# Performance work log

Measured on AMD Instinct MI355X. Metric: run time of the kernel, lower is better.

The kernel has to match this reference:

```python
import jax, jax.numpy as jnp
import numpy as np

N_NODES = 50000
NUM_REL = 8
IN_DIM = 128
HID = 256
NUM_CLASSES = 2
E = 1600000
M = 200000
LN_EPS = 1e-5


def setup_inputs() -> dict:
    key = jax.random.key(0)
    ks = jax.random.split(key, 20)
    s = 0.05
    inp = {
        "x": jax.random.normal(ks[0], (N_NODES, IN_DIM), jnp.float32),
        "edge_index": jax.random.randint(ks[1], (2, E), 0, N_NODES, jnp.int32),
        "edge_type": jax.random.randint(ks[2], (E,), 0, NUM_REL, jnp.int32),
        "dec_edges": jax.random.randint(ks[3], (M, 2), 0, N_NODES, jnp.int32),
        # conv1
        "W1": jax.random.normal(ks[4], (NUM_REL, IN_DIM, HID), jnp.float32) * s,
        "root1": jax.random.normal(ks[5], (IN_DIM, HID), jnp.float32) * s,
        "b1": jnp.zeros((HID,), jnp.float32),
        # conv2
        "W2": jax.random.normal(ks[6], (NUM_REL, HID, HID), jnp.float32) * s,
        "root2": jax.random.normal(ks[7], (HID, HID), jnp.float32) * s,
        "b2": jnp.zeros((HID,), jnp.float32),
        # layernorms
        "ln1_g": jnp.ones((HID,), jnp.float32),
        "ln1_b": jnp.zeros((HID,), jnp.float32),
        "ln2_g": jnp.ones((HID,), jnp.float32),
        "ln2_b": jnp.zeros((HID,), jnp.float32),
        # edge MLP: 2*HID -> HID -> HID//2 -> NUM_CLASSES
        "mlp_w1": jax.random.normal(ks[8], (2 * HID, HID), jnp.float32) * s,
        "mlp_b1": jnp.zeros((HID,), jnp.float32),
        "mlp_w2": jax.random.normal(ks[9], (HID, HID // 2), jnp.float32) * s,
        "mlp_b2": jnp.zeros((HID // 2,), jnp.float32),
        "mlp_w3": jax.random.normal(ks[10], (HID // 2, NUM_CLASSES), jnp.float32) * s,
        "mlp_b3": jnp.zeros((NUM_CLASSES,), jnp.float32),
    }
    return inp


def layer_norm(h, g, b):
    mu = jnp.mean(h, axis=-1, keepdims=True)
    var = jnp.mean(jnp.square(h - mu), axis=-1, keepdims=True)
    return (h - mu) * jax.lax.rsqrt(var + LN_EPS) * g + b


def rgcn_conv(x, edge_index, edge_type, W, root, bias):
    # PyG RGCNConv with aggr='mean': per-relation mean aggregation of
    # neighbor features, aggregate-then-transform (valid since linear),
    # plus root transform and bias.
    src, dst = edge_index[0], edge_index[1]
    xs = x[src]  # [E, d_in]
    out = x @ root + bias
    num_rel = W.shape[0]
    for r in range(num_rel):
        m = (edge_type == r).astype(x.dtype)  # [E]
        agg = jax.ops.segment_sum(xs * m[:, None], dst, num_segments=x.shape[0])
        cnt = jax.ops.segment_sum(m, dst, num_segments=x.shape[0])
        out = out + (agg / jnp.maximum(cnt, 1.0)[:, None]) @ W[r]
    return out


def reference(x, edge_index, edge_type, dec_edges,
              W1, root1, b1, W2, root2, b2,
              ln1_g, ln1_b, ln2_g, ln2_b,
              mlp_w1, mlp_b1, mlp_w2, mlp_b2, mlp_w3, mlp_b3):
    # encode (dropout is identity in eval mode)
    h1 = rgcn_conv(x, edge_index, edge_type, W1, root1, b1)
    h1 = layer_norm(jax.nn.relu(h1), ln1_g, ln1_b)
    h2 = rgcn_conv(h1, edge_index, edge_type, W2, root2, b2)
    h2 = layer_norm(jax.nn.relu(h2), ln2_g, ln2_b)
    h = h1 + h2
    # decode: gather endpoints, concat, MLP (exact-erf GELU as nn.GELU)
    z = jnp.concatenate([h[dec_edges[:, 0]], h[dec_edges[:, 1]]], axis=1)
    z = jax.nn.gelu(z @ mlp_w1 + mlp_b1, approximate=False)
    z = jax.nn.gelu(z @ mlp_w2 + mlp_b2, approximate=False)
    return z @ mlp_w3 + mlp_b3
```

## Files before the change

### kernel.cpp

```cpp
#include <hip/hip_runtime.h>
#include <math.h>

typedef __attribute__((ext_vector_type(8))) short short8;
typedef __attribute__((ext_vector_type(4))) float f32x4;
typedef __attribute__((address_space(3))) void lds_void;
typedef const __attribute__((address_space(1))) void glb_void;

#define N_NODES 50000
#define NUM_REL 8
#define IN_DIM 128
#define HID 256
#define E_EDGES 1600000
#define M_DEC 200000
#define K1 1152
#define K2 2304
#define LN_EPS 1e-5f
#define NSEG (N_NODES * 8)
#define NB2 782
#define SA_WG 391
#define SA_CH 4096
#define SA_DCH 512

__device__ __forceinline__ float b2f(ushort u) {
    union { unsigned int i; float f; } v; v.i = ((unsigned int)u) << 16; return v.f;
}
__device__ __forceinline__ ushort f2b(float f) {
    union { float f; unsigned int i; } v; v.f = f;
    unsigned int r = v.i + 0x7FFFu + ((v.i >> 16) & 1u);
    return (ushort)(r >> 16);
}
__device__ __forceinline__ unsigned int pk2(ushort a, ushort b) {
    return (unsigned int)a | ((unsigned int)b << 16);
}
__device__ __forceinline__ float gelu_fast(float x) {
    float y = 1.5957691216f * (x + 0.044715f * x * x * x);
    float e = __expf(y);
    float t = 1.f - 2.f * __builtin_amdgcn_rcpf(e + 1.f);
    return 0.5f * x * (1.f + t);
}
__device__ __forceinline__ int clampn(int v) {
    if ((unsigned)v >= N_NODES) v = (v < 0) ? 0 : N_NODES - 1;
    return v;
}


__global__ __launch_bounds__(256) void coarse_count(const int* __restrict__ ei,
                                                    const int* __restrict__ dec,
                                                    int* __restrict__ bh, int* __restrict__ dh) {
    __shared__ int lb[NB2], ld[NB2];
    const int t = threadIdx.x;
    for (int i = t; i < NB2; i += 256) { lb[i] = 0; ld[i] = 0; }
    __syncthreads();
    const int e0 = blockIdx.x * SA_CH;
#pragma unroll
    for (int k = 0; k < 16; ++k) {
        int e = e0 + k * 256 + t;
        if (e < E_EDGES) {
            int dst = clampn(ei[E_EDGES + e]);
            atomicAdd(&lb[dst >> 6], 1);
        }
    }
    const int d0 = blockIdx.x * SA_DCH;
#pragma unroll
    for (int k = 0; k < 2; ++k) {
        int i = d0 + k * 256 + t;
        if (i < M_DEC) {
            int a = clampn(dec[(size_t)i * 2]);
            atomicAdd(&ld[a >> 6], 1);
        }
    }
    __syncthreads();
    for (int i = t; i < NB2; i += 256) {
        if (lb[i]) atomicAdd(&bh[i], lb[i]);
        if (ld[i]) atomicAdd(&dh[i], ld[i]);
    }
}

__global__ __launch_bounds__(1024) void scan_buckets(const int* __restrict__ bh, int* __restrict__ bbase,
                                                     int* __restrict__ bcur,
                                                     const int* __restrict__ dh, int* __restrict__ dbase,
                                                     int* __restrict__ dcur, int* __restrict__ rp2) {
    __shared__ int ts[1024];
    const int t = threadIdx.x;
    const int* src = (blockIdx.x == 0) ? bh : dh;
    int* ob = (blockIdx.x == 0) ? bbase : dbase;
    int* oc = (blockIdx.x == 0) ? bcur : dcur;
    int v = (t < NB2) ? src[t] : 0;
    ts[t] = v;
    __syncthreads();
#pragma unroll
    for (int off = 1; off < 1024; off <<= 1) {
        int u = (t >= off) ? ts[t - off] : 0;
        __syncthreads();
        ts[t] += u;
        __syncthreads();
    }
    if (t < NB2) { int ex = ts[t] - v; ob[t] = ex; oc[t] = ex; }
    if (t == NB2 - 1) ob[NB2] = ts[t];
    if (t == 0 && blockIdx.x == 0) rp2[NSEG] = E_EDGES;
}

__global__ __launch_bounds__(256) void stageA(const int* __restrict__ ei, const int* __restrict__ et,
                                              int* __restrict__ bcur, unsigned int* __restrict__ sbuf,
                                              const int* __restrict__ dec, int* __restrict__ dcur,
                                              int* __restrict__ perm) {
    __shared__ int h[NB2], base_[NB2];
    const int t = threadIdx.x;
    const int e0 = blockIdx.x * SA_CH;
    for (int i = t; i < NB2; i += 256) h[i] = 0;
    __syncthreads();
    int myb[16];
#pragma unroll
    for (int k = 0; k < 16; ++k) {
        int e = e0 + k * 256 + t;
        int b = -1;
        if (e < E_EDGES) {
            int dst = clampn(ei[E_EDGES + e]);
            b = dst >> 6;
            atomicAdd(&h[b], 1);
        }
        myb[k] = b;
    }
    __syncthreads();
    for (int i = t; i < NB2; i += 256) {
        int c = h[i];
        base_[i] = c ? atomicAdd(&bcur[i], c) : 0;
    }
    __syncthreads();
    for (int i = t; i < NB2; i += 256) h[i] = 0;
    __syncthreads();
#pragma unroll
    for (int k = 0; k < 16; ++k) {
        int e = e0 + k * 256 + t;
        int b = myb[k];
        if (b >= 0) {
            int dst = clampn(ei[E_EDGES + e]);
            int src = clampn(ei[e]);
            int r = et[e] & 7;
            int off = atomicAdd(&h[b], 1);
            sbuf[base_[b] + off] =
                (unsigned)src | ((unsigned)r << 16) | ((unsigned)(dst & 63) << 19);
        }
    }
    __syncthreads();
    for (int i = t; i < NB2; i += 256) h[i] = 0;
    __syncthreads();
    const int d0 = blockIdx.x * SA_DCH;
    int dbk[2];
#pragma unroll
    for (int k = 0; k < 2; ++k) {
        int i = d0 + k * 256 + t;
        int b = -1;
        if (i < M_DEC) {
            int a = clampn(dec[(size_t)i * 2]);
            b = a >> 6;
            atomicAdd(&h[b], 1);
        }
        dbk[k] = b;
    }
    __syncthreads();
    for (int i = t; i < NB2; i += 256) {
        int c = h[i];
        base_[i] = c ? atomicAdd(&dcur[i], c) : 0;
    }
    __syncthreads();
    for (int i = t; i < NB2; i += 256) h[i] = 0;
    __syncthreads();
#pragma unroll
    for (int k = 0; k < 2; ++k) {
        int i = d0 + k * 256 + t;
        int b = dbk[k];
        if (b >= 0) {
            int off = atomicAdd(&h[b], 1);
            perm[base_[b] + off] = i;
        }
    }
}

__global__ __launch_bounds__(512) void stageB(const unsigned int* __restrict__ sbuf,
                                              const int* __restrict__ bbase,
                                              int* __restrict__ rp2,
                                              unsigned int* __restrict__ epk) {
    __shared__ int cnt[512];
    __shared__ int pref[512];
    const int t = threadIdx.x;
    const int b = blockIdx.x;
    const int s0 = bbase[b], s1 = bbase[b + 1];
    cnt[t] = 0;
    __syncthreads();
    for (int i = s0 + t; i < s1; i += 512) {
        unsigned int p = sbuf[i];
        int ls = (((p >> 19) & 63) << 3) | ((p >> 16) & 7);
        atomicAdd(&cnt[ls], 1);
    }
    __syncthreads();
    pref[t] = cnt[t];
    __syncthreads();
#pragma unroll
    for (int off = 1; off < 512; off <<= 1) {
        int u = (t >= off) ? pref[t - off] : 0;
        __syncthreads();
        pref[t] += u;
        __syncthreads();
    }
    int excl = pref[t] - cnt[t];
    int seg = b * 512 + t;
    if (seg < NSEG) rp2[seg] = s0 + excl;
    __syncthreads();
    pref[t] = excl;
    cnt[t] = 0;
    __syncthreads();
    for (int i = s0 + t; i < s1; i += 512) {
        unsigned int p = sbuf[i];
        int ls = (((p >> 19) & 63) << 3) | ((p >> 16) & 7);
        int off = atomicAdd(&cnt[ls], 1);
        epk[s0 + pref[ls] + off] = p & 0xFFFFu;
    }
}

__global__ void pack_all(const float* __restrict__ x, ushort* __restrict__ xb,
                         const float* __restrict__ root1, const float* __restrict__ W1,
                         const float* __restrict__ root2, const float* __restrict__ W2,
                         ushort* __restrict__ B1t, ushort* __restrict__ B2t,
                         const float* __restrict__ mw1, const float* __restrict__ mw2,
                         ushort* __restrict__ wuvt, ushort* __restrict__ w2t) {
    const int XC = N_NODES * IN_DIM / 4;
    const int N1 = HID * K1;
    const int N2 = HID * K2;
    const int NU = 512 * 256;
    const int NW = 128 * 256;
    int idx = blockIdx.x * 256 + threadIdx.x;
    if (idx < XC) {
        float4 v = *(const float4*)(x + (size_t)idx * 4);
        uint2 o;
        o.x = pk2(f2b(v.x), f2b(v.y));
        o.y = pk2(f2b(v.z), f2b(v.w));
        *(uint2*)(xb + (size_t)idx * 4) = o;
        return;
    }
    idx -= XC;
    if (idx < N1) {
        int n = idx / K1, k = idx % K1;
        float v;
        if (k < IN_DIM) v = root1[k * HID + n];
        else { int kk = k - IN_DIM; v = W1[(size_t)(kk >> 7) * IN_DIM * HID + (kk & 127) * HID + n]; }
        B1t[(size_t)n * K1 + k] = f2b(v);
        return;
    }
    idx -= N1;
    if (idx < N2) {
        int n = idx / K2, k = idx % K2;
        float v;
        if (k < HID) v = root2[k * HID + n];
        else { int kk = k - HID; v = W2[(size_t)(kk >> 8) * HID * HID + (kk & 255) * HID + n]; }
        B2t[(size_t)n * K2 + k] = f2b(v);
        return;
    }
    idx -= N2;
    if (idx < NU) {
        int n = idx / 256, k = idx % 256;
        float v = (n < 256) ? mw1[(size_t)k * 256 + n] : mw1[(size_t)(256 + k) * 256 + (n - 256)];
        wuvt[(size_t)n * 256 + k] = f2b(v);
        return;
    }
    idx -= NU;
    if (idx < NW) {
        int n = idx / 256, k = idx % 256;
        w2t[n * 256 + k] = f2b(mw2[k * 128 + n]);
    }
}


#define FL1() { int c_ = segend - segbeg; float inv_ = c_ > 0 ? 1.f / (float)c_ : 0.f; \
    *(unsigned int*)(Arow + IN_DIM + r * IN_DIM + 2 * lane) = \
        pk2(f2b((aA.x + aB.x) * inv_), f2b((aA.y + aB.y) * inv_)); \
    aA.x = 0.f; aA.y = 0.f; aB.x = 0.f; aB.y = 0.f; \
    ++r; segbeg = segend; segend = (r < 8) ? rp[r + 1] : end; \
    if (segend < segbeg) segend = segbeg; if (segend > end) segend = end; }
#define CK1(EI) { while (r < 8 && (EI) >= segend) FL1(); }
#define AC1A(U) { aA.x += b2f((ushort)((U) & 0xFFFFu)); aA.y += b2f((ushort)((U) >> 16)); }
#define AC1B(U) { aB.x += b2f((ushort)((U) & 0xFFFFu)); aB.y += b2f((ushort)((U) >> 16)); }

__global__ __launch_bounds__(256) void agg1_kernel(const ushort* __restrict__ xb,
                                                   const int* __restrict__ rp2,
                                                   const unsigned int* __restrict__ epk,
                                                   ushort* __restrict__ Achunk, int n0, int m) {
    const int w = threadIdx.x >> 6, lane = threadIdx.x & 63;
    const int local = blockIdx.x * 4 + w;
    if (local >= m) return;
    const int n = n0 + local;
    const int* rp = rp2 + n * 8;
    ushort* Arow = Achunk + (size_t)local * K1;
    const ushort* xbb = xb + 2 * lane;
    *(unsigned int*)(Arow + 2 * lane) = *(const unsigned int*)(xb + (size_t)n * IN_DIM + 2 * lane);

    int beg = rp[0], end = rp[8];
    if (beg < 0) beg = 0;
    if (end > E_EDGES) end = E_EDGES;
    if (end < beg) end = beg;

    float2 aA = {0.f, 0.f}, aB = {0.f, 0.f};
    int r = 0, segbeg = beg, segend = rp[1];
    if (segend < segbeg) segend = segbeg; if (segend > end) segend = end;

    int e = beg;
    for (; e + 7 < end; e += 8) {
        unsigned int p0 = epk[e],     p1 = epk[e + 1], p2 = epk[e + 2], p3 = epk[e + 3];
        unsigned int p4 = epk[e + 4], p5 = epk[e + 5], p6 = epk[e + 6], p7 = epk[e + 7];
        unsigned int u0 = *(const unsigned int*)(xbb + (size_t)p0 * IN_DIM);
        unsigned int u1 = *(const unsigned int*)(xbb + (size_t)p1 * IN_DIM);
        unsigned int u2 = *(const unsigned int*)(xbb + (size_t)p2 * IN_DIM);
        unsigned int u3 = *(const unsigned int*)(xbb + (size_t)p3 * IN_DIM);
        unsigned int u4 = *(const unsigned int*)(xbb + (size_t)p4 * IN_DIM);
        unsigned int u5 = *(const unsigned int*)(xbb + (size_t)p5 * IN_DIM);
        unsigned int u6 = *(const unsigned int*)(xbb + (size_t)p6 * IN_DIM);
        unsigned int u7 = *(const unsigned int*)(xbb + (size_t)p7 * IN_DIM);
        CK1(e)     AC1A(u0) CK1(e + 1) AC1B(u1)
        CK1(e + 2) AC1A(u2) CK1(e + 3) AC1B(u3)
        CK1(e + 4) AC1A(u4) CK1(e + 5) AC1B(u5)
        CK1(e + 6) AC1A(u6) CK1(e + 7) AC1B(u7)
    }
    for (; e < end; ++e) {
        unsigned int p = epk[e];
        unsigned int u = *(const unsigned int*)(xbb + (size_t)p * IN_DIM);
        CK1(e) AC1A(u)
    }
    while (r < 8) FL1();
}

#define FL2() { int c_ = segend - segbeg; float inv_ = c_ > 0 ? 1.f / (float)c_ : 0.f; \
    f32x4 t_ = aA + aB; uint2 o_; \
    o_.x = pk2(f2b(t_[0] * inv_), f2b(t_[1] * inv_)); \
    o_.y = pk2(f2b(t_[2] * inv_), f2b(t_[3] * inv_)); \
    *(uint2*)(Arow + HID + r * HID + 4 * lane) = o_; \
    aA = (f32x4){0.f, 0.f, 0.f, 0.f}; aB = aA; \
    ++r; segbeg = segend; segend = (r < 8) ? rp[r + 1] : end; \
    if (segend < segbeg) segend = segbeg; if (segend > end) segend = end; }
#define CK2(EI) { while (r < 8 && (EI) >= segend) FL2(); }
#define AC2A(U) { f32x4 f_; \
    f_[0] = b2f((ushort)((U).x & 0xFFFFu)); f_[1] = b2f((ushort)((U).x >> 16)); \
    f_[2] = b2f((ushort)((U).y & 0xFFFFu)); f_[3] = b2f((ushort)((U).y >> 16)); aA += f_; }
#define AC2B(U) { f32x4 f_; \
    f_[0] = b2f((ushort)((U).x & 0xFFFFu)); f_[1] = b2f((ushort)((U).x >> 16)); \
    f_[2] = b2f((ushort)((U).y & 0xFFFFu)); f_[3] = b2f((ushort)((U).y >> 16)); aB += f_; }

__global__ __launch_bounds__(256) void agg2_kernel(const ushort* __restrict__ h1,
                                                   const int* __restrict__ rp2,
                                                   const unsigned int* __restrict__ epk,
                                                   ushort* __restrict__ Achunk, int n0, int m) {
    const int w = threadIdx.x >> 6, lane = threadIdx.x & 63;
    const int local = blockIdx.x * 4 + w;
    if (local >= m) return;
    const int n = n0 + local;
    const int* rp = rp2 + n * 8;
    ushort* Arow = Achunk + (size_t)local * K2;
    const ushort* hb = h1 + 4 * lane;
    *(uint2*)(Arow + 4 * lane) = *(const uint2*)(h1 + (size_t)n * HID + 4 * lane);

    int beg = rp[0], end = rp[8];
    if (beg < 0) beg = 0;
    if (end > E_EDGES) end = E_EDGES;
    if (end < beg) end = beg;

    f32x4 aA = {0.f, 0.f, 0.f, 0.f}, aB = {0.f, 0.f, 0.f, 0.f};
    int r = 0, segbeg = beg, segend = rp[1];
    if (segend < segbeg) segend = segbeg; if (segend > end) segend = end;

    int e = beg;
    for (; e + 7 < end; e += 8) {
        unsigned int p0 = epk[e],     p1 = epk[e + 1], p2 = epk[e + 2], p3 = epk[e + 3];
        unsigned int p4 = epk[e + 4], p5 = epk[e + 5], p6 = epk[e + 6], p7 = epk[e + 7];
        uint2 u0 = *(const uint2*)(hb + (size_t)p0 * HID);
        uint2 u1 = *(const uint2*)(hb + (size_t)p1 * HID);
        uint2 u2 = *(const uint2*)(hb + (size_t)p2 * HID);
        uint2 u3 = *(const uint2*)(hb + (size_t)p3 * HID);
        uint2 u4 = *(const uint2*)(hb + (size_t)p4 * HID);
        uint2 u5 = *(const uint2*)(hb + (size_t)p5 * HID);
        uint2 u6 = *(const uint2*)(hb + (size_t)p6 * HID);
        uint2 u7 = *(const uint2*)(hb + (size_t)p7 * HID);
        CK2(e)     AC2A(u0) CK2(e + 1) AC2B(u1)
        CK2(e + 2) AC2A(u2) CK2(e + 3) AC2B(u3)
        CK2(e + 4) AC2A(u4) CK2(e + 5) AC2B(u5)
        CK2(e + 6) AC2A(u6) CK2(e + 7) AC2B(u7)
    }
    for (; e < end; ++e) {
        unsigned int p = epk[e];
        uint2 u = *(const uint2*)(hb + (size_t)p * HID);
        CK2(e) AC2A(u)
    }
    while (r < 8) FL2();
}


#define STAGE(BUF, KO) { \
    __builtin_amdgcn_global_load_lds((glb_void*)(Ab + (KO)), \
        (lds_void*)(AsBase + (BUF) * 4096 + wave * 8 * 64), 16, 0, 0); \
    _Pragma("unroll") \
    for (int j_ = 0; j_ < 4; ++j_) \
        __builtin_amdgcn_global_load_lds((glb_void*)(Bb + (size_t)j_ * 8 * K + (KO)), \
            (lds_void*)(BsBase + (BUF) * 16384 + (wave * 32 + j_ * 8) * 64), 16, 0, 0); }

#define COMPUTE(CUR) { \
    _Pragma("unroll") \
    for (int kk = 0; kk < 2; ++kk) { \
        const int gsw = (((kk * 4 + qd) ^ (cc & 7)) * 8); \
        short8 af[2], bfv[4]; \
        _Pragma("unroll") \
        for (int i = 0; i < 2; ++i) \
            af[i] = *(const short8*)&AsBase[(CUR) * 4096 + (mh * 32 + i * 16 + cc) * 64 + gsw]; \
        _Pragma("unroll") \
        for (int j = 0; j < 4; ++j) \
            bfv[j] = *(const short8*)&BsBase[(CUR) * 16384 + (wn + j * 16 + cc) * 64 + gsw]; \
        _Pragma("unroll") \
        for (int i = 0; i < 2; ++i) \
            _Pragma("unroll") \
            for (int j = 0; j < 4; ++j) \
                acc[i][j] = __builtin_amdgcn_mfma_f32_16x16x32_bf16(af[i], bfv[j], acc[i][j], 0, 0, 0); \
    } }

__global__ __launch_bounds__(512, 4) void gemm_fused(
    const ushort* __restrict__ A, const ushort* __restrict__ Bt,
    int lda, int M, int K,
    const float* __restrict__ bias, const float* __restrict__ g,
    const float* __restrict__ bvec, const ushort* __restrict__ resid,
    ushort* __restrict__ outp, int ldc, int rowOff) {
    __shared__ __align__(16) ushort smem[40960];
    ushort* AsBase = smem;
    ushort* BsBase = smem + 2 * 64 * 64;
    const int tid = threadIdx.x;
    const int wave = tid >> 6, lane = tid & 63;
    const int w4 = wave & 3, mh = wave >> 2;
    const int cc = lane & 15, qd = lane >> 4;
    const int row0 = blockIdx.x * 64;
    const int colBase = blockIdx.y * 256;
    const int wn = w4 * 64;
    const int srow = lane >> 3;
    const int sgrp = (lane & 7) ^ (srow & 7);
    f32x4 acc[2][4];
#pragma unroll
    for (int i = 0; i < 2; ++i)
#pragma unroll
        for (int j = 0; j < 4; ++j) acc[i][j] = (f32x4){0.f, 0.f, 0.f, 0.f};

    const ushort* Ab = A + (size_t)(row0 + wave * 8 + srow) * lda + sgrp * 8;
    const ushort* Bb = Bt + (size_t)(colBase + wave * 32 + srow) * K + sgrp * 8;

    STAGE(0, 0)
    for (int k0 = 0; k0 < K; k0 += 128) {
        if (k0 + 64 < K) {
            STAGE(1, k0 + 64)
            asm volatile("s_waitcnt vmcnt(5)" ::: "memory");
        } else {
            asm volatile("s_waitcnt vmcnt(0)" ::: "memory");
        }
        __builtin_amdgcn_s_barrier();
        COMPUTE(0)
        asm volatile("s_waitcnt lgkmcnt(0)" ::: "memory");
        __builtin_amdgcn_s_barrier();

        if (k0 + 128 < K) {
            STAGE(0, k0 + 128)
            asm volatile("s_waitcnt vmcnt(5)" ::: "memory");
        } else {
            asm volatile("s_waitcnt vmcnt(0)" ::: "memory");
        }
        __builtin_amdgcn_s_barrier();
        COMPUTE(1)
        asm volatile("s_waitcnt lgkmcnt(0)" ::: "memory");
        __builtin_amdgcn_s_barrier();
    }

    if (g) {
        float* partS = (float*)smem;
        float* partQ = (float*)smem + 256;
        float* muS   = (float*)smem + 512;
        float* rsS   = (float*)smem + 576;
#pragma unroll
        for (int j = 0; j < 4; ++j) {
            float bcol = bias[wn + j * 16 + cc];
#pragma unroll
            for (int i = 0; i < 2; ++i)
#pragma unroll
                for (int r = 0; r < 4; ++r)
                    acc[i][j][r] = fmaxf(acc[i][j][r] + bcol, 0.f);
        }
#pragma unroll
        for (int i = 0; i < 2; ++i)
#pragma unroll
            for (int r = 0; r < 4; ++r) {
                float s = acc[i][0][r] + acc[i][1][r] + acc[i][2][r] + acc[i][3][r];
                float q = acc[i][0][r] * acc[i][0][r] + acc[i][1][r] * acc[i][1][r]
                        + acc[i][2][r] * acc[i][2][r] + acc[i][3][r] * acc[i][3][r];
#pragma unroll
                for (int off = 1; off <= 8; off <<= 1) {
                    s += __shfl_xor(s, off, 64);
                    q += __shfl_xor(q, off, 64);
                }
                if (cc == 0) {
                    int row = mh * 32 + i * 16 + qd * 4 + r;
                    partS[row * 4 + w4] = s;
                    partQ[row * 4 + w4] = q;
                }
            }
        __syncthreads();
        if (tid < 64) {
            float S = partS[tid * 4] + partS[tid * 4 + 1] + partS[tid * 4 + 2] + partS[tid * 4 + 3];
            float Q = partQ[tid * 4] + partQ[tid * 4 + 1] + partQ[tid * 4 + 2] + partQ[tid * 4 + 3];
            float mu = S * (1.f / 256.f);
            float var = Q * (1.f / 256.f) - mu * mu;
            muS[tid] = mu;
            rsS[tid] = rsqrtf(fmaxf(var, 0.f) + LN_EPS);
        }
        __syncthreads();
#pragma unroll
        for (int i = 0; i < 2; ++i)
#pragma unroll
            for (int r = 0; r < 4; ++r) {
                int row = mh * 32 + i * 16 + qd * 4 + r;
                int grow = row0 + row;
                if (grow >= M) continue;
                float mu = muS[row], rs = rsS[row];
                size_t base = (size_t)(rowOff + grow) * ldc;
#pragma unroll
                for (int j = 0; j < 4; ++j) {
                    int col = wn + j * 16 + cc;
                    float val = (acc[i][j][r] - mu) * rs * g[col] + bvec[col];
                    if (resid) val += b2f(resid[base + col]);
                    outp[base + col] = f2b(val);
                }
            }
    } else {
#pragma unroll
        for (int i = 0; i < 2; ++i)
#pragma unroll
            for (int r = 0; r < 4; ++r) {
                int grow = row0 + mh * 32 + i * 16 + qd * 4 + r;
                if (grow >= M) continue;
                size_t base = (size_t)(rowOff + grow) * ldc;
#pragma unroll
                for (int j = 0; j < 4; ++j) {
                    int col = colBase + wn + j * 16 + cc;
                    outp[base + col] = f2b(acc[i][j][r]);
                }
            }
    }
}

__global__ __launch_bounds__(256) void edge_kernel(
    const ushort* __restrict__ uv, const int* __restrict__ dec, const int* __restrict__ perm,
    const float* __restrict__ b1, const ushort* __restrict__ w2t,
    const float* __restrict__ b2, const float* __restrict__ w3,
    const float* __restrict__ b3, float* __restrict__ outp, int M) {
    __shared__ __align__(16) ushort z1s[64][264];
    __shared__ __align__(16) ushort z2s[64][136];
    __shared__ float b1s[256], b2s[128], w3s[256];
    const int tid = threadIdx.x;
    const int wave = tid >> 6, lane = tid & 63;
    const int cc = lane & 15, qd = lane >> 4, lk = qd * 8, rr = qd * 4;
    const int e0 = blockIdx.x * 64;

    b1s[tid] = b1[tid];
    if (tid < 128) b2s[tid] = b2[tid];
    w3s[tid] = w3[tid];
    __syncthreads();

    {
        int e = tid >> 2, seg = tid & 3;
        int ge = perm[e0 + e];
        if (ge < 0) ge = 0; if (ge >= M) ge = M - 1;
        int a = dec[(size_t)ge * 2];
        int b = dec[(size_t)ge * 2 + 1];
        if (a < 0) a = 0; if (a >= N_NODES) a = N_NODES - 1;
        if (b < 0) b = 0; if (b >= N_NODES) b = N_NODES - 1;
        const ushort* up = uv + (size_t)a * 512 + seg * 64;
        const ushort* vp = uv + (size_t)b * 512 + 256 + seg * 64;
        short8 us[8], vs[8];
#pragma unroll
        for (int j = 0; j < 8; ++j) us[j] = *(const short8*)(up + j * 8);
#pragma unroll
        for (int j = 0; j < 8; ++j) vs[j] = *(const short8*)(vp + j * 8);
        int d0 = seg * 64;
#pragma unroll
        for (int j = 0; j < 8; ++j) {
            int d = d0 + j * 8;
            short8 zs;
#pragma unroll
            for (int l = 0; l < 8; ++l) {
                float z = b2f((ushort)us[j][l]) + b2f((ushort)vs[j][l]) + b1s[d + l];
                zs[l] = (short)f2b(gelu_fast(z));
            }
            *(short8*)&z1s[e][d] = zs;
        }
    }
    __syncthreads();

    f32x4 acc[4][2];
#pragma unroll
    for (int i = 0; i < 4; ++i)
#pragma unroll
        for (int j = 0; j < 2; ++j) acc[i][j] = (f32x4){0.f, 0.f, 0.f, 0.f};
    const int n0 = wave * 32;
#pragma unroll
    for (int ks = 0; ks < 8; ++ks) {
        short8 af[4], bfv[2];
#pragma unroll
        for (int i = 0; i < 4; ++i) af[i] = *(const short8*)&z1s[i * 16 + cc][ks * 32 + lk];
#pragma unroll
        for (int j = 0; j < 2; ++j)
            bfv[j] = *(const short8*)(w2t + (size_t)(n0 + j * 16 + cc) * 256 + ks * 32 + lk);
#pragma unroll
        for (int i = 0; i < 4; ++i)
#pragma unroll
            for (int j = 0; j < 2; ++j)
                acc[i][j] = __builtin_amdgcn_mfma_f32_16x16x32_bf16(af[i], bfv[j], acc[i][j], 0, 0, 0);
    }
#pragma unroll
    for (int i = 0; i < 4; ++i)
#pragma unroll
        for (int j = 0; j < 2; ++j)
#pragma unroll
            for (int r = 0; r < 4; ++r) {
                int m = i * 16 + rr + r;
                int n = n0 + j * 16 + cc;
                z2s[m][n] = f2b(gelu_fast(acc[i][j][r] + b2s[n]));
            }
    __syncthreads();

    if (tid < 128) {
        int e = tid >> 1, c = tid & 1;
        float s = b3[c];
        for (int k = 0; k < 128; ++k) s += b2f(z2s[e][k]) * w3s[k * 2 + c];
        int ge = perm[e0 + e];
        if (ge >= 0 && ge < M) outp[(size_t)ge * 2 + c] = s;
    }
}

extern "C" void kernel_launch(void* const* d_in, const int* in_sizes, int n_in,
                              void* d_out, int out_size, void* d_ws, size_t ws_size,
                              hipStream_t stream) {
    const float* x          = (const float*)d_in[0];
    const int*   edge_index = (const int*)d_in[1];
    const int*   edge_type  = (const int*)d_in[2];
    const int*   dec_edges  = (const int*)d_in[3];
    const float* W1         = (const float*)d_in[4];
    const float* root1      = (const float*)d_in[5];
    const float* b1         = (const float*)d_in[6];
    const float* W2         = (const float*)d_in[7];
    const float* root2      = (const float*)d_in[8];
    const float* b2         = (const float*)d_in[9];
    const float* ln1_g      = (const float*)d_in[10];
    const float* ln1_b      = (const float*)d_in[11];
    const float* ln2_g      = (const float*)d_in[12];
    const float* ln2_b      = (const float*)d_in[13];
    const float* mlp_w1     = (const float*)d_in[14];
    const float* mlp_b1     = (const float*)d_in[15];
    const float* mlp_w2     = (const float*)d_in[16];
    const float* mlp_b2     = (const float*)d_in[17];
    const float* mlp_w3     = (const float*)d_in[18];
    const float* mlp_b3     = (const float*)d_in[19];

    char* ws = (char*)d_ws;
    size_t off = 0;
    auto alloc = [&](size_t bytes) {
        void* p = ws + off;
        off += (bytes + 255) & ~(size_t)255;
        return p;
    };
    unsigned int* epk     = (unsigned int*)alloc((size_t)E_EDGES * 4);
    unsigned int* sbuf    = (unsigned int*)alloc((size_t)E_EDGES * 4);
    int*          rp2     = (int*)alloc((size_t)(NSEG + 1) * 4);
    int*          hz      = (int*)alloc((size_t)2 * NB2 * 4);
    int*          bh      = hz;
    int*          dh      = hz + NB2;
    int*          bbase   = (int*)alloc((size_t)(NB2 + 1) * 4);
    int*          dbase   = (int*)alloc((size_t)(NB2 + 1) * 4);
    int*          bcur    = (int*)alloc((size_t)NB2 * 4);
    int*          dcur    = (int*)alloc((size_t)NB2 * 4);
    int*          perm    = (int*)alloc((size_t)M_DEC * 4);
    ushort*       B1t     = (ushort*)alloc((size_t)HID * K1 * 2);
    ushort*       B2t     = (ushort*)alloc((size_t)HID * K2 * 2);
    ushort*       wuvt    = (ushort*)alloc((size_t)512 * 256 * 2);
    ushort*       w2t     = (ushort*)alloc((size_t)128 * 256 * 2);
    ushort*       xb      = (ushort*)alloc((size_t)N_NODES * IN_DIM * 2);
    ushort*       hfin    = (ushort*)alloc((size_t)N_NODES * HID * 2);

    size_t regionOff = off;
    ushort* h1ln  = (ushort*)(ws + regionOff);
    ushort* uvbuf = h1ln;
    size_t h1b = (((size_t)N_NODES * HID * 2) + 255) & ~(size_t)255;
    ushort* Achunk = (ushort*)(ws + regionOff + h1b);
    long long chunkB = (long long)ws_size - (long long)(regionOff + h1b);
    int chunk = 64;
    if (chunkB > 0) {
        long long c = chunkB / ((long long)K2 * 2);
        if (c > N_NODES) c = N_NODES;
        c &= ~63LL;
        if (c >= 64) chunk = (int)c;
    }
    int chunk1 = chunk * 2;
    if (chunk1 > N_NODES) chunk1 = N_NODES;

    hipMemsetAsync(hz, 0, (size_t)2 * NB2 * 4, stream);
    coarse_count<<<SA_WG, 256, 0, stream>>>(edge_index, dec_edges, bh, dh);
    scan_buckets<<<2, 1024, 0, stream>>>(bh, bbase, bcur, dh, dbase, dcur, rp2);
    stageA<<<SA_WG, 256, 0, stream>>>(edge_index, edge_type, bcur, sbuf, dec_edges, dcur, perm);
    stageB<<<NB2, 512, 0, stream>>>(sbuf, bbase, rp2, epk);

    {
        int total = N_NODES * IN_DIM / 4 + HID * K1 + HID * K2 + 512 * 256 + 128 * 256;
        pack_all<<<(total + 255) / 256, 256, 0, stream>>>(x, xb, root1, W1, root2, W2,
                                                          B1t, B2t, mlp_w1, mlp_w2, wuvt, w2t);
    }

    for (int n0 = 0; n0 < N_NODES; n0 += chunk1) {
        int m = N_NODES - n0; if (m > chunk1) m = chunk1;
        agg1_kernel<<<(m + 3) / 4, 256, 0, stream>>>(xb, rp2, epk, Achunk, n0, m);
        gemm_fused<<<dim3((m + 63) / 64, 1), 512, 0, stream>>>(
            Achunk, B1t, K1, m, K1, b1, ln1_g, ln1_b, nullptr, h1ln, HID, n0);
    }
    for (int n0 = 0; n0 < N_NODES; n0 += chunk) {
        int m = N_NODES - n0; if (m > chunk) m = chunk;
        agg2_kernel<<<(m + 3) / 4, 256, 0, stream>>>(h1ln, rp2, epk, Achunk, n0, m);
        gemm_fused<<<dim3((m + 63) / 64, 1), 512, 0, stream>>>(
            Achunk, B2t, K2, m, K2, b2, ln2_g, ln2_b, h1ln, hfin, HID, n0);
    }

    gemm_fused<<<dim3((N_NODES + 63) / 64, 2), 512, 0, stream>>>(
        hfin, wuvt, HID, N_NODES, HID, nullptr, nullptr, nullptr, nullptr, uvbuf, 512, 0);

    edge_kernel<<<(M_DEC + 63) / 64, 256, 0, stream>>>(
        uvbuf, dec_edges, perm, mlp_b1, w2t, mlp_b2, mlp_w3, mlp_b3, (float*)d_out, M_DEC);
}
```

Baseline: 704.3 us.

## Triple-buffer GEMM K-loop and widen gather unroll in aggregation kernels

The fused GEMM moves from a double-buffered to a triple-buffered LDS pipeline. Two K-tiles are prefetched ahead of compute, with the wait threshold raised to match, and the launch-bounds occupancy hint drops from 4 to 2. Both aggregation kernels get a 16-wide gather unroll ahead of the existing 8-wide loop, plus an occupancy hint of 6, to keep more neighbour loads in flight. The trade-off is that the GEMM's shared memory grows to about 120 KB per block, which likely allows only one resident block per CU. That cuts the latency hiding that came from running several blocks at once, and the larger unroll raises register pressure in the aggregation kernels.

```diff
diff --git a/kernel.cpp b/kernel.cpp
--- a/kernel.cpp
+++ b/kernel.cpp
@@ -281,10 +281,10 @@
 #define AC1A(U) { aA.x += b2f((ushort)((U) & 0xFFFFu)); aA.y += b2f((ushort)((U) >> 16)); }
 #define AC1B(U) { aB.x += b2f((ushort)((U) & 0xFFFFu)); aB.y += b2f((ushort)((U) >> 16)); }
 
-__global__ __launch_bounds__(256) void agg1_kernel(const ushort* __restrict__ xb,
-                                                   const int* __restrict__ rp2,
-                                                   const unsigned int* __restrict__ epk,
-                                                   ushort* __restrict__ Achunk, int n0, int m) {
+__global__ __launch_bounds__(256, 6) void agg1_kernel(const ushort* __restrict__ xb,
+                                                      const int* __restrict__ rp2,
+                                                      const unsigned int* __restrict__ epk,
+                                                      ushort* __restrict__ Achunk, int n0, int m) {
     const int w = threadIdx.x >> 6, lane = threadIdx.x & 63;
     const int local = blockIdx.x * 4 + w;
     if (local >= m) return;
@@ -304,6 +304,36 @@
     if (segend < segbeg) segend = segbeg; if (segend > end) segend = end;
 
     int e = beg;
+    for (; e + 15 < end; e += 16) {
+        unsigned int p0 = epk[e],      p1 = epk[e + 1],  p2 = epk[e + 2],  p3 = epk[e + 3];
+        unsigned int p4 = epk[e + 4],  p5 = epk[e + 5],  p6 = epk[e + 6],  p7 = epk[e + 7];
+        unsigned int p8 = epk[e + 8],  p9 = epk[e + 9],  pa = epk[e + 10], pb = epk[e + 11];
+        unsigned int pc = epk[e + 12], pd = epk[e + 13], pe = epk[e + 14], pf = epk[e + 15];
+        unsigned int u0 = *(const unsigned int*)(xbb + (size_t)p0 * IN_DIM);
+        unsigned int u1 = *(const unsigned int*)(xbb + (size_t)p1 * IN_DIM);
+        unsigned int u2 = *(const unsigned int*)(xbb + (size_t)p2 * IN_DIM);
+        unsigned int u3 = *(const unsigned int*)(xbb + (size_t)p3 * IN_DIM);
+        unsigned int u4 = *(const unsigned int*)(xbb + (size_t)p4 * IN_DIM);
+        unsigned int u5 = *(const unsigned int*)(xbb + (size_t)p5 * IN_DIM);
+        unsigned int u6 = *(const unsigned int*)(xbb + (size_t)p6 * IN_DIM);
+        unsigned int u7 = *(const unsigned int*)(xbb + (size_t)p7 * IN_DIM);
+        unsigned int u8 = *(const unsigned int*)(xbb + (size_t)p8 * IN_DIM);
+        unsigned int u9 = *(const unsigned int*)(xbb + (size_t)p9 * IN_DIM);
+        unsigned int ua = *(const unsigned int*)(xbb + (size_t)pa * IN_DIM);
+        unsigned int ub = *(const unsigned int*)(xbb + (size_t)pb * IN_DIM);
+        unsigned int uc = *(const unsigned int*)(xbb + (size_t)pc * IN_DIM);
+        unsigned int ud = *(const unsigned int*)(xbb + (size_t)pd * IN_DIM);
+        unsigned int ue = *(const unsigned int*)(xbb + (size_t)pe * IN_DIM);
+        unsigned int uf = *(const unsigned int*)(xbb + (size_t)pf * IN_DIM);
+        CK1(e)      AC1A(u0) CK1(e + 1)  AC1B(u1)
+        CK1(e + 2)  AC1A(u2) CK1(e + 3)  AC1B(u3)
+        CK1(e + 4)  AC1A(u4) CK1(e + 5)  AC1B(u5)
+        CK1(e + 6)  AC1A(u6) CK1(e + 7)  AC1B(u7)
+        CK1(e + 8)  AC1A(u8) CK1(e + 9)  AC1B(u9)
+        CK1(e + 10) AC1A(ua) CK1(e + 11) AC1B(ub)
+        CK1(e + 12) AC1A(uc) CK1(e + 13) AC1B(ud)
+        CK1(e + 14) AC1A(ue) CK1(e + 15) AC1B(uf)
+    }
     for (; e + 7 < end; e += 8) {
         unsigned int p0 = epk[e],     p1 = epk[e + 1], p2 = epk[e + 2], p3 = epk[e + 3];
         unsigned int p4 = epk[e + 4], p5 = epk[e + 5], p6 = epk[e + 6], p7 = epk[e + 7];
@@ -344,10 +374,10 @@
     f_[0] = b2f((ushort)((U).x & 0xFFFFu)); f_[1] = b2f((ushort)((U).x >> 16)); \
     f_[2] = b2f((ushort)((U).y & 0xFFFFu)); f_[3] = b2f((ushort)((U).y >> 16)); aB += f_; }
 
-__global__ __launch_bounds__(256) void agg2_kernel(const ushort* __restrict__ h1,
-                                                   const int* __restrict__ rp2,
-                                                   const unsigned int* __restrict__ epk,
-                                                   ushort* __restrict__ Achunk, int n0, int m) {
+__global__ __launch_bounds__(256, 6) void agg2_kernel(const ushort* __restrict__ h1,
+                                                      const int* __restrict__ rp2,
+                                                      const unsigned int* __restrict__ epk,
+                                                      ushort* __restrict__ Achunk, int n0, int m) {
     const int w = threadIdx.x >> 6, lane = threadIdx.x & 63;
     const int local = blockIdx.x * 4 + w;
     if (local >= m) return;
@@ -367,6 +397,36 @@
     if (segend < segbeg) segend = segbeg; if (segend > end) segend = end;
 
     int e = beg;
+    for (; e + 15 < end; e += 16) {
+        unsigned int p0 = epk[e],      p1 = epk[e + 1],  p2 = epk[e + 2],  p3 = epk[e + 3];
+        unsigned int p4 = epk[e + 4],  p5 = epk[e + 5],  p6 = epk[e + 6],  p7 = epk[e + 7];
+        unsigned int p8 = epk[e + 8],  p9 = epk[e + 9],  pa = epk[e + 10], pb = epk[e + 11];
+        unsigned int pc = epk[e + 12], pd = epk[e + 13], pe = epk[e + 14], pf = epk[e + 15];
+        uint2 u0 = *(const uint2*)(hb + (size_t)p0 * HID);
+        uint2 u1 = *(const uint2*)(hb + (size_t)p1 * HID);
+        uint2 u2 = *(const uint2*)(hb + (size_t)p2 * HID);
+        uint2 u3 = *(const uint2*)(hb + (size_t)p3 * HID);
+        uint2 u4 = *(const uint2*)(hb + (size_t)p4 * HID);
+        uint2 u5 = *(const uint2*)(hb + (size_t)p5 * HID);
+        uint2 u6 = *(const uint2*)(hb + (size_t)p6 * HID);
+        uint2 u7 = *(const uint2*)(hb + (size_t)p7 * HID);
+        uint2 u8 = *(const uint2*)(hb + (size_t)p8 * HID);
+        uint2 u9 = *(const uint2*)(hb + (size_t)p9 * HID);
+        uint2 ua = *(const uint2*)(hb + (size_t)pa * HID);
+        uint2 ub = *(const uint2*)(hb + (size_t)pb * HID);
+        uint2 uc = *(const uint2*)(hb + (size_t)pc * HID);
+        uint2 ud = *(const uint2*)(hb + (size_t)pd * HID);
+        uint2 ue = *(const uint2*)(hb + (size_t)pe * HID);
+        uint2 uf = *(const uint2*)(hb + (size_t)pf * HID);
+        CK2(e)      AC2A(u0) CK2(e + 1)  AC2B(u1)
+        CK2(e + 2)  AC2A(u2) CK2(e + 3)  AC2B(u3)
+        CK2(e + 4)  AC2A(u4) CK2(e + 5)  AC2B(u5)
+        CK2(e + 6)  AC2A(u6) CK2(e + 7)  AC2B(u7)
+        CK2(e + 8)  AC2A(u8) CK2(e + 9)  AC2B(u9)
+        CK2(e + 10) AC2A(ua) CK2(e + 11) AC2B(ub)
+        CK2(e + 12) AC2A(uc) CK2(e + 13) AC2B(ud)
+        CK2(e + 14) AC2A(ue) CK2(e + 15) AC2B(uf)
+    }
     for (; e + 7 < end; e += 8) {
         unsigned int p0 = epk[e],     p1 = epk[e + 1], p2 = epk[e + 2], p3 = epk[e + 3];
         unsigned int p4 = epk[e + 4], p5 = epk[e + 5], p6 = epk[e + 6], p7 = epk[e + 7];
@@ -418,15 +478,27 @@
                 acc[i][j] = __builtin_amdgcn_mfma_f32_16x16x32_bf16(af[i], bfv[j], acc[i][j], 0, 0, 0); \
     } }
 
-__global__ __launch_bounds__(512, 4) void gemm_fused(
+#define PHASE(BUF, KCUR, KPRE) { \
+    if ((KPRE) < K) { \
+        STAGE(((BUF) + 2) % 3, (KPRE)) \
+        asm volatile("s_waitcnt vmcnt(10)" ::: "memory"); \
+    } else { \
+        asm volatile("s_waitcnt vmcnt(0)" ::: "memory"); \
+    } \
+    __builtin_amdgcn_s_barrier(); \
+    COMPUTE(BUF) \
+    asm volatile("s_waitcnt lgkmcnt(0)" ::: "memory"); \
+    __builtin_amdgcn_s_barrier(); }
+
+__global__ __launch_bounds__(512, 2) void gemm_fused(
     const ushort* __restrict__ A, const ushort* __restrict__ Bt,
     int lda, int M, int K,
     const float* __restrict__ bias, const float* __restrict__ g,
     const float* __restrict__ bvec, const ushort* __restrict__ resid,
     ushort* __restrict__ outp, int ldc, int rowOff) {
-    __shared__ __align__(16) ushort smem[40960];
+    __shared__ __align__(16) ushort smem[61440];
     ushort* AsBase = smem;
-    ushort* BsBase = smem + 2 * 64 * 64;
+    ushort* BsBase = smem + 3 * 64 * 64;
     const int tid = threadIdx.x;
     const int wave = tid >> 6, lane = tid & 63;
     const int w4 = wave & 3, mh = wave >> 2;
@@ -446,28 +518,13 @@
     const ushort* Bb = Bt + (size_t)(colBase + wave * 32 + srow) * K + sgrp * 8;
 
     STAGE(0, 0)
-    for (int k0 = 0; k0 < K; k0 += 128) {
-        if (k0 + 64 < K) {
-            STAGE(1, k0 + 64)
-            asm volatile("s_waitcnt vmcnt(5)" ::: "memory");
-        } else {
-            asm volatile("s_waitcnt vmcnt(0)" ::: "memory");
-        }
-        __builtin_amdgcn_s_barrier();
-        COMPUTE(0)
-        asm volatile("s_waitcnt lgkmcnt(0)" ::: "memory");
-        __builtin_amdgcn_s_barrier();
-
-        if (k0 + 128 < K) {
-            STAGE(0, k0 + 128)
-            asm volatile("s_waitcnt vmcnt(5)" ::: "memory");
-        } else {
-            asm volatile("s_waitcnt vmcnt(0)" ::: "memory");
-        }
-        __builtin_amdgcn_s_barrier();
-        COMPUTE(1)
-        asm volatile("s_waitcnt lgkmcnt(0)" ::: "memory");
-        __builtin_amdgcn_s_barrier();
+    if (64 < K) STAGE(1, 64)
+    for (int k0 = 0; k0 < K; k0 += 192) {
+        PHASE(0, k0, k0 + 128)
+        if (k0 + 64 >= K) break;
+        PHASE(1, k0 + 64, k0 + 192)
+        if (k0 + 128 >= K) break;
+        PHASE(2, k0 + 128, k0 + 256)
     }
 
     if (g) {
```

Result: slower. 746.8 us (+6.0%).

## Overlap next-chunk aggregation with current-chunk GEMM in one fused launch

Applied to the files above, without the earlier changes.

The aggregation and GEMM paths are split into device functions. A combined kernel now assigns its first blocks to the GEMM on the current chunk and its remaining blocks to aggregating the next chunk into a second buffer, so memory-bound gathers run alongside MFMA work. Chunk size is capped and the workspace is double-buffered. Launch bounds for the GEMM drop from 4 to 2 blocks per CU, which loosens register limits but may reduce occupancy. The fused kernel also carries a larger shared allocation into the aggregation blocks.

```diff
diff --git a/kernel.cpp b/kernel.cpp
--- a/kernel.cpp
+++ b/kernel.cpp
@@ -281,16 +281,11 @@
 #define AC1A(U) { aA.x += b2f((ushort)((U) & 0xFFFFu)); aA.y += b2f((ushort)((U) >> 16)); }
 #define AC1B(U) { aB.x += b2f((ushort)((U) & 0xFFFFu)); aB.y += b2f((ushort)((U) >> 16)); }
 
-__global__ __launch_bounds__(256) void agg1_kernel(const ushort* __restrict__ xb,
-                                                   const int* __restrict__ rp2,
-                                                   const unsigned int* __restrict__ epk,
-                                                   ushort* __restrict__ Achunk, int n0, int m) {
-    const int w = threadIdx.x >> 6, lane = threadIdx.x & 63;
-    const int local = blockIdx.x * 4 + w;
-    if (local >= m) return;
-    const int n = n0 + local;
+__device__ __forceinline__ void agg1_node(const ushort* __restrict__ xb,
+                                          const int* __restrict__ rp2,
+                                          const unsigned int* __restrict__ epk,
+                                          ushort* __restrict__ Arow, int n, int lane) {
     const int* rp = rp2 + n * 8;
-    ushort* Arow = Achunk + (size_t)local * K1;
     const ushort* xbb = xb + 2 * lane;
     *(unsigned int*)(Arow + 2 * lane) = *(const unsigned int*)(xb + (size_t)n * IN_DIM + 2 * lane);
 
@@ -344,16 +339,11 @@
     f_[0] = b2f((ushort)((U).x & 0xFFFFu)); f_[1] = b2f((ushort)((U).x >> 16)); \
     f_[2] = b2f((ushort)((U).y & 0xFFFFu)); f_[3] = b2f((ushort)((U).y >> 16)); aB += f_; }
 
-__global__ __launch_bounds__(256) void agg2_kernel(const ushort* __restrict__ h1,
-                                                   const int* __restrict__ rp2,
-                                                   const unsigned int* __restrict__ epk,
-                                                   ushort* __restrict__ Achunk, int n0, int m) {
-    const int w = threadIdx.x >> 6, lane = threadIdx.x & 63;
-    const int local = blockIdx.x * 4 + w;
-    if (local >= m) return;
-    const int n = n0 + local;
+__device__ __forceinline__ void agg2_node(const ushort* __restrict__ h1,
+                                          const int* __restrict__ rp2,
+                                          const unsigned int* __restrict__ epk,
+                                          ushort* __restrict__ Arow, int n, int lane) {
     const int* rp = rp2 + n * 8;
-    ushort* Arow = Achunk + (size_t)local * K2;
     const ushort* hb = h1 + 4 * lane;
     *(uint2*)(Arow + 4 * lane) = *(const uint2*)(h1 + (size_t)n * HID + 4 * lane);
 
@@ -389,6 +379,26 @@
         CK2(e) AC2A(u)
     }
     while (r < 8) FL2();
+}
+
+__global__ __launch_bounds__(256) void agg1_kernel(const ushort* __restrict__ xb,
+                                                   const int* __restrict__ rp2,
+                                                   const unsigned int* __restrict__ epk,
+                                                   ushort* __restrict__ Achunk, int n0, int m) {
+    const int w = threadIdx.x >> 6, lane = threadIdx.x & 63;
+    const int local = blockIdx.x * 4 + w;
+    if (local >= m) return;
+    agg1_node(xb, rp2, epk, Achunk + (size_t)local * K1, n0 + local, lane);
+}
+
+__global__ __launch_bounds__(256) void agg2_kernel(const ushort* __restrict__ h1,
+                                                   const int* __restrict__ rp2,
+                                                   const unsigned int* __restrict__ epk,
+                                                   ushort* __restrict__ Achunk, int n0, int m) {
+    const int w = threadIdx.x >> 6, lane = threadIdx.x & 63;
+    const int local = blockIdx.x * 4 + w;
+    if (local >= m) return;
+    agg2_node(h1, rp2, epk, Achunk + (size_t)local * K2, n0 + local, lane);
 }
 
 
@@ -418,21 +428,20 @@
                 acc[i][j] = __builtin_amdgcn_mfma_f32_16x16x32_bf16(af[i], bfv[j], acc[i][j], 0, 0, 0); \
     } }
 
-__global__ __launch_bounds__(512, 4) void gemm_fused(
+__device__ __forceinline__ void gemm_body(
+    ushort* smem,
     const ushort* __restrict__ A, const ushort* __restrict__ Bt,
     int lda, int M, int K,
     const float* __restrict__ bias, const float* __restrict__ g,
     const float* __restrict__ bvec, const ushort* __restrict__ resid,
-    ushort* __restrict__ outp, int ldc, int rowOff) {
-    __shared__ __align__(16) ushort smem[40960];
+    ushort* __restrict__ outp, int ldc, int rowOff, int colBase, int bx) {
     ushort* AsBase = smem;
     ushort* BsBase = smem + 2 * 64 * 64;
     const int tid = threadIdx.x;
     const int wave = tid >> 6, lane = tid & 63;
     const int w4 = wave & 3, mh = wave >> 2;
     const int cc = lane & 15, qd = lane >> 4;
-    const int row0 = blockIdx.x * 64;
-    const int colBase = blockIdx.y * 256;
+    const int row0 = bx * 64;
     const int wn = w4 * 64;
     const int srow = lane >> 3;
     const int sgrp = (lane & 7) ^ (srow & 7);
@@ -543,6 +552,42 @@
                     outp[base + col] = f2b(acc[i][j][r]);
                 }
             }
+    }
+}
+
+__global__ __launch_bounds__(512, 2) void gemm_fused(
+    const ushort* __restrict__ A, const ushort* __restrict__ Bt,
+    int lda, int M, int K,
+    const float* __restrict__ bias, const float* __restrict__ g,
+    const float* __restrict__ bvec, const ushort* __restrict__ resid,
+    ushort* __restrict__ outp, int ldc, int rowOff) {
+    __shared__ __align__(16) ushort smem[40960];
+    gemm_body(smem, A, Bt, lda, M, K, bias, g, bvec, resid, outp, ldc, rowOff,
+              blockIdx.y * 256, blockIdx.x);
+}
+
+__global__ __launch_bounds__(512, 2) void fused_ga(
+    const ushort* __restrict__ A, const ushort* __restrict__ Bt,
+    int lda, int M, int K,
+    const float* __restrict__ bias, const float* __restrict__ g,
+    const float* __restrict__ bvec, const ushort* __restrict__ resid,
+    ushort* __restrict__ outp, int ldc, int rowOff, int gemmBlocks,
+    int aggKind, const ushort* __restrict__ gsrc,
+    const int* __restrict__ rp2, const unsigned int* __restrict__ epk,
+    ushort* __restrict__ Anext, int n0n, int mn) {
+    __shared__ __align__(16) ushort smem[40960];
+    if ((int)blockIdx.x < gemmBlocks) {
+        gemm_body(smem, A, Bt, lda, M, K, bias, g, bvec, resid, outp, ldc, rowOff,
+                  0, blockIdx.x);
+    } else {
+        const int bid = (int)blockIdx.x - gemmBlocks;
+        const int w = threadIdx.x >> 6, lane = threadIdx.x & 63;
+        const int local = bid * 8 + w;
+        if (local >= mn) return;
+        if (aggKind == 1)
+            agg1_node(gsrc, rp2, epk, Anext + (size_t)local * lda, n0n + local, lane);
+        else
+            agg2_node(gsrc, rp2, epk, Anext + (size_t)local * lda, n0n + local, lane);
     }
 }
 
@@ -688,17 +733,14 @@
     ushort* h1ln  = (ushort*)(ws + regionOff);
     ushort* uvbuf = h1ln;
     size_t h1b = (((size_t)N_NODES * HID * 2) + 255) & ~(size_t)255;
-    ushort* Achunk = (ushort*)(ws + regionOff + h1b);
-    long long chunkB = (long long)ws_size - (long long)(regionOff + h1b);
-    int chunk = 64;
-    if (chunkB > 0) {
-        long long c = chunkB / ((long long)K2 * 2);
-        if (c > N_NODES) c = N_NODES;
-        c &= ~63LL;
-        if (c >= 64) chunk = (int)c;
-    }
-    int chunk1 = chunk * 2;
-    if (chunk1 > N_NODES) chunk1 = N_NODES;
+
+    long long avail = (long long)ws_size - (long long)(regionOff + h1b);
+    long long cmax = (avail > 0) ? avail / (2LL * K2 * 2) : 64;
+    int C = (int)((cmax > 12544) ? 12544 : cmax);
+    C &= ~63;
+    if (C < 64) C = 64;
+    ushort* buf0 = (ushort*)(ws + regionOff + h1b);
+    ushort* buf1 = buf0 + (size_t)C * K2;
 
     hipMemsetAsync(hz, 0, (size_t)2 * NB2 * 4, stream);
     coarse_count<<<SA_WG, 256, 0, stream>>>(edge_index, dec_edges, bh, dh);
@@ -712,18 +754,31 @@
                                                           B1t, B2t, mlp_w1, mlp_w2, wuvt, w2t);
     }
 
-    for (int n0 = 0; n0 < N_NODES; n0 += chunk1) {
-        int m = N_NODES - n0; if (m > chunk1) m = chunk1;
-        agg1_kernel<<<(m + 3) / 4, 256, 0, stream>>>(xb, rp2, epk, Achunk, n0, m);
-        gemm_fused<<<dim3((m + 63) / 64, 1), 512, 0, stream>>>(
-            Achunk, B1t, K1, m, K1, b1, ln1_g, ln1_b, nullptr, h1ln, HID, n0);
-    }
-    for (int n0 = 0; n0 < N_NODES; n0 += chunk) {
-        int m = N_NODES - n0; if (m > chunk) m = chunk;
-        agg2_kernel<<<(m + 3) / 4, 256, 0, stream>>>(h1ln, rp2, epk, Achunk, n0, m);
-        gemm_fused<<<dim3((m + 63) / 64, 1), 512, 0, stream>>>(
-            Achunk, B2t, K2, m, K2, b2, ln2_g, ln2_b, h1ln, hfin, HID, n0);
-    }
+    auto run_conv = [&](int aggKind, const ushort* gsrc, const ushort* Bt, int Kdim,
+                        const float* bias, const float* lg, const float* lb,
+                        const ushort* resid, ushort* outp) {
+        int nch = (N_NODES + C - 1) / C;
+        int m0 = (C < N_NODES) ? C : N_NODES;
+        if (aggKind == 1)
+            agg1_kernel<<<(m0 + 3) / 4, 256, 0, stream>>>(gsrc, rp2, epk, buf0, 0, m0);
+        else
+            agg2_kernel<<<(m0 + 3) / 4, 256, 0, stream>>>(gsrc, rp2, epk, buf0, 0, m0);
+        for (int i = 0; i < nch; ++i) {
+            int n0 = i * C;
+            int mi = N_NODES - n0; if (mi > C) mi = C;
+            int gb = (mi + 63) / 64;
+            int n0n = (i + 1) * C;
+            int mn = (i + 1 < nch) ? (N_NODES - n0n > C ? C : N_NODES - n0n) : 0;
+            int ab = (mn + 7) / 8;
+            ushort* curb = (i & 1) ? buf1 : buf0;
+            ushort* nxtb = (i & 1) ? buf0 : buf1;
+            fused_ga<<<gb + ab, 512, 0, stream>>>(curb, Bt, Kdim, mi, Kdim, bias, lg, lb,
+                                                  resid, outp, HID, n0, gb,
+                                                  aggKind, gsrc, rp2, epk, nxtb, n0n, mn);
+        }
+    };
+    run_conv(1, xb, B1t, K1, b1, ln1_g, ln1_b, nullptr, h1ln);
+    run_conv(2, h1ln, B2t, K2, b2, ln2_g, ln2_b, h1ln, hfin);
 
     gemm_fused<<<dim3((N_NODES + 63) / 64, 2), 512, 0, stream>>>(
         hfin, wuvt, HID, N_NODES, HID, nullptr, nullptr, nullptr, nullptr, uvbuf, 512, 0);
```

After: 759.9 us. +7.9%, slower.
